# Performance work log

Hardware: AMD Instinct MI355X
Metric: run time of the kernel (lower is better)

## Reference

```python
import jax, jax.numpy as jnp
import numpy as np

H = 128  # hidden_size
I = 28   # input_size
C = 10   # num_classes


def setup_inputs() -> dict:
    key = jax.random.key(0)
    ks = jax.random.split(key, 11)
    s = 1.0 / np.sqrt(H)  # torch nn.RNN init scale
    return {
        "x": jax.random.normal(ks[0], (8192, 28, I), dtype=jnp.float32),
        "W_ih0": jax.random.uniform(ks[1], (H, I), jnp.float32, -s, s),
        "W_hh0": jax.random.uniform(ks[2], (H, H), jnp.float32, -s, s),
        "b_ih0": jax.random.uniform(ks[3], (H,), jnp.float32, -s, s),
        "b_hh0": jax.random.uniform(ks[4], (H,), jnp.float32, -s, s),
        "W_ih1": jax.random.uniform(ks[5], (H, H), jnp.float32, -s, s),
        "W_hh1": jax.random.uniform(ks[6], (H, H), jnp.float32, -s, s),
        "b_ih1": jax.random.uniform(ks[7], (H,), jnp.float32, -s, s),
        "b_hh1": jax.random.uniform(ks[8], (H,), jnp.float32, -s, s),
        "fc_w": jax.random.uniform(ks[9], (C, H), jnp.float32, -s, s),
        "fc_b": jax.random.uniform(ks[10], (C,), jnp.float32, -s, s),
    }


def _rnn_layer_full(x, W_ih, b_ih, W_hh, b_hh):
    # x: [B, T, D] -> full output sequence [B, T, H]
    B = x.shape[0]
    h0 = jnp.zeros((B, H), x.dtype)
    xw = jnp.einsum('btd,hd->bth', x, W_ih) + b_ih  # precompute input GEMM

    def step(h, xw_t):
        h = jnp.tanh(xw_t + h @ W_hh.T + b_hh)
        return h, h

    _, ys = jax.lax.scan(step, h0, jnp.swapaxes(xw, 0, 1))  # [T, B, H]
    return jnp.swapaxes(ys, 0, 1)


def _rnn_layer_last(x, W_ih, b_ih, W_hh, b_hh):
    # only the final hidden state is needed downstream
    B = x.shape[0]
    h0 = jnp.zeros((B, H), x.dtype)
    xw = jnp.einsum('btd,hd->bth', x, W_ih) + b_ih

    def step(h, xw_t):
        h = jnp.tanh(xw_t + h @ W_hh.T + b_hh)
        return h, None

    h_last, _ = jax.lax.scan(step, h0, jnp.swapaxes(xw, 0, 1))
    return h_last


def reference(x, W_ih0, W_hh0, b_ih0, b_hh0, W_ih1, W_hh1, b_ih1, b_hh1, fc_w, fc_b):
    out0 = _rnn_layer_full(x, W_ih0, b_ih0, W_hh0, b_hh0)   # [B, T, H]
    h_last = _rnn_layer_last(out0, W_ih1, b_ih1, W_hh1, b_hh1)  # [B, H] == out[:, -1, :]
    return h_last @ fc_w.T + fc_b  # [B, C]
```

## Files before the change

### kernel.cpp

```cpp
#include <hip/hip_runtime.h>

#define HSZ 128
#define ISZ 28
#define TSZ 28
#define CSZ 10
#define BT  32
#define NG  2
#define NT  384

typedef _Float16 half_t;
typedef _Float16 v8h __attribute__((ext_vector_type(8)));
typedef _Float16 v4h __attribute__((ext_vector_type(4)));
typedef float v4f __attribute__((ext_vector_type(4)));

__device__ __forceinline__ float fast_tanh(float x) {
    float e = __expf(2.f * x);
    return 1.f - 2.f * __builtin_amdgcn_rcpf(e + 1.f);
}
__device__ __forceinline__ int imin(int a, int b) { return a < b ? a : b; }

__global__ __launch_bounds__(NT, 2)
void rnn_ws(const float* __restrict__ x,
            const float* __restrict__ W_ih0, const float* __restrict__ W_hh0,
            const float* __restrict__ b_ih0, const float* __restrict__ b_hh0,
            const float* __restrict__ W_ih1, const float* __restrict__ W_hh1,
            const float* __restrict__ b_ih1, const float* __restrict__ b_hh1,
            const float* __restrict__ fc_w, const float* __restrict__ fc_b,
            float* __restrict__ out)
{
    __shared__ half_t xs[TSZ][NG][512];
    __shared__ half_t h0r[4][NG][2048];
    __shared__ half_t h1r[4][NG][2048];
    __shared__ int    flags[8];

    const int tid  = threadIdx.x;
    const int wave = tid >> 6;
    const int lane = tid & 63;
    const int ln   = lane & 15;
    const int quad = lane >> 4;
    const int b0   = blockIdx.x * BT;
    const int ro   = lane * 8;
    const int wbq  = (quad >> 1) * 128 + ln * 8 + (quad & 1) * 4;
    volatile int* vf = (volatile int*)flags;

    for (int it = 0; it < 10; ++it) {
        const int c = tid + it * NT;
        if (c < TSZ * 128) {
            const int q = c & 3;
            const int n = (c >> 2) & 15;
            const int g = (c >> 6) & 1;
            const int t = c >> 7;
            const float* gp = x + ((size_t)(b0 + g * 16 + n) * TSZ + t) * ISZ + q * 8;
            float4 a = *(const float4*)gp;
            float4 b = (q < 3) ? *(const float4*)(gp + 4) : make_float4(1.f, 0.f, 0.f, 0.f);
            v8h p = {(half_t)a.x, (half_t)a.y, (half_t)a.z, (half_t)a.w,
                     (half_t)b.x, (half_t)b.y, (half_t)b.z, (half_t)b.w};
            *(v8h*)&xs[t][g][(q * 16 + n) * 8] = p;
        }
    }
    {
        const v8h z = {(half_t)0.f, (half_t)0.f, (half_t)0.f, (half_t)0.f,
                       (half_t)0.f, (half_t)0.f, (half_t)0.f, (half_t)0.f};
        for (int idx = tid; idx < 512; idx += NT) {
            *(v8h*)&h0r[3][0][idx * 8] = z;
            *(v8h*)&h1r[3][0][idx * 8] = z;
        }
        if (tid < 8) flags[tid] = 0;
    }
    __syncthreads();

    if (wave < NG) {
        const int g = wave;
        v8h aWx[8], aW0[8][4];
#pragma unroll
        for (int rt = 0; rt < 8; ++rt) {
            const int row = rt * 16 + ln;
            const float bias = b_ih0[row] + b_hh0[row];
            const float* pw = W_ih0 + row * ISZ + quad * 8;
            float4 a = *(const float4*)pw;
            float4 b = (quad < 3) ? *(const float4*)(pw + 4)
                                  : make_float4(bias, 0.f, 0.f, 0.f);
            aWx[rt] = (v8h){(half_t)a.x, (half_t)a.y, (half_t)a.z, (half_t)a.w,
                            (half_t)b.x, (half_t)b.y, (half_t)b.z, (half_t)b.w};
#pragma unroll
            for (int ks = 0; ks < 4; ++ks) {
                const float4* p0 = (const float4*)(W_hh0 + row * HSZ + ks * 32 + quad * 8);
                float4 c = p0[0], d = p0[1];
                aW0[rt][ks] = (v8h){(half_t)c.x, (half_t)c.y, (half_t)c.z, (half_t)c.w,
                                    (half_t)d.x, (half_t)d.y, (half_t)d.z, (half_t)d.w};
            }
        }
        __builtin_amdgcn_s_setprio(1);

        for (int t = 0; t < TSZ; ++t) {
            if (t >= 4) {
                while (imin(vf[2 + 2 * g], vf[3 + 2 * g]) < t - 3)
                    __builtin_amdgcn_s_sleep(1);
            }
            __asm__ volatile("" ::: "memory");
            const int sr = (t + 3) & 3, sw = t & 3;

            v8h bh[4];
#pragma unroll
            for (int ks = 0; ks < 4; ++ks)
                bh[ks] = *(const v8h*)&h0r[sr][g][ks * 512 + ro];
            const v8h bx = *(const v8h*)&xs[t][g][ro];

            v4f acc[8];
#pragma unroll
            for (int rt = 0; rt < 8; ++rt)
                acc[rt] = __builtin_amdgcn_mfma_f32_16x16x32_f16(
                    aWx[rt], bx, (v4f){0.f, 0.f, 0.f, 0.f}, 0, 0, 0);
#pragma unroll
            for (int ks = 0; ks < 4; ++ks)
#pragma unroll
                for (int rt = 0; rt < 8; ++rt)
                    acc[rt] = __builtin_amdgcn_mfma_f32_16x16x32_f16(
                        aW0[rt][ks], bh[ks], acc[rt], 0, 0, 0);
#pragma unroll
            for (int rt = 0; rt < 8; ++rt) {
                v4h p = {(half_t)fast_tanh(acc[rt][0]), (half_t)fast_tanh(acc[rt][1]),
                         (half_t)fast_tanh(acc[rt][2]), (half_t)fast_tanh(acc[rt][3])};
                *(v4h*)&h0r[sw][g][(rt >> 1) * 512 + (rt & 1) * 256 + wbq] = p;
            }
            __asm__ volatile("s_waitcnt lgkmcnt(0)" ::: "memory");
            if (lane == 0) vf[g] = t + 1;
        }
        __builtin_amdgcn_s_setprio(0);
    } else {
        const int q4 = wave - 2;
        const int g  = q4 >> 1;
        const int c  = q4 & 1;
        v8h aW1i[4][4], aW1h[4][4];
        v4f bias1[4];
#pragma unroll
        for (int rt = 0; rt < 4; ++rt) {
            const int row = c * 64 + rt * 16 + ln;
            float4 p = *(const float4*)(b_ih1 + c * 64 + rt * 16 + quad * 4);
            float4 q = *(const float4*)(b_hh1 + c * 64 + rt * 16 + quad * 4);
            bias1[rt] = (v4f){p.x + q.x, p.y + q.y, p.z + q.z, p.w + q.w};
#pragma unroll
            for (int ks = 0; ks < 4; ++ks) {
                const float4* p1 = (const float4*)(W_ih1 + row * HSZ + ks * 32 + quad * 8);
                const float4* p2 = (const float4*)(W_hh1 + row * HSZ + ks * 32 + quad * 8);
                float4 a = p1[0], b = p1[1];
                aW1i[rt][ks] = (v8h){(half_t)a.x, (half_t)a.y, (half_t)a.z, (half_t)a.w,
                                     (half_t)b.x, (half_t)b.y, (half_t)b.z, (half_t)b.w};
                a = p2[0]; b = p2[1];
                aW1h[rt][ks] = (v8h){(half_t)a.x, (half_t)a.y, (half_t)a.z, (half_t)a.w,
                                     (half_t)b.x, (half_t)b.y, (half_t)b.z, (half_t)b.w};
            }
        }

        for (int t = 0; t < TSZ; ++t) {
            const int pid = 2 + 2 * g + (c ^ 1);
            while (vf[g] < t + 1 || vf[pid] < t)
                __builtin_amdgcn_s_sleep(1);
            __asm__ volatile("" ::: "memory");
            const int s0 = t & 3, s1 = (t + 3) & 3;

            v8h bh0[4], bh1[4];
#pragma unroll
            for (int ks = 0; ks < 4; ++ks) {
                bh0[ks] = *(const v8h*)&h0r[s0][g][ks * 512 + ro];
                bh1[ks] = *(const v8h*)&h1r[s1][g][ks * 512 + ro];
            }
            v4f si[4], sh[4];
#pragma unroll
            for (int rt = 0; rt < 4; ++rt) {
                si[rt] = bias1[rt];
                sh[rt] = (v4f){0.f, 0.f, 0.f, 0.f};
            }
#pragma unroll
            for (int ks = 0; ks < 4; ++ks)
#pragma unroll
                for (int rt = 0; rt < 4; ++rt) {
                    si[rt] = __builtin_amdgcn_mfma_f32_16x16x32_f16(
                        aW1i[rt][ks], bh0[ks], si[rt], 0, 0, 0);
                    sh[rt] = __builtin_amdgcn_mfma_f32_16x16x32_f16(
                        aW1h[rt][ks], bh1[ks], sh[rt], 0, 0, 0);
                }
#pragma unroll
            for (int rt = 0; rt < 4; ++rt) {
                const v4f a1 = si[rt] + sh[rt];
                const int rtg = c * 4 + rt;
                v4h p = {(half_t)fast_tanh(a1[0]), (half_t)fast_tanh(a1[1]),
                         (half_t)fast_tanh(a1[2]), (half_t)fast_tanh(a1[3])};
                *(v4h*)&h1r[s0][g][(rtg >> 1) * 512 + (rtg & 1) * 256 + wbq] = p;
            }
            __asm__ volatile("s_waitcnt lgkmcnt(0)" ::: "memory");
            if (lane == 0) vf[2 + 2 * g + c] = t + 1;
        }
    }
    __syncthreads();

    if (tid < BT * CSZ) {
        const int m = tid / CSZ, cc = tid - m * CSZ;
        const int g = m >> 4, n = m & 15;
        float s = fc_b[cc];
#pragma unroll
        for (int ks = 0; ks < 4; ++ks) {
#pragma unroll
            for (int q2 = 0; q2 < 4; ++q2) {
                const v8h hv = *(const v8h*)&h1r[3][g][(ks * 64 + q2 * 16 + n) * 8];
                const int kb = ks * 32 + q2 * 8;
                const float4 w0 = *(const float4*)(fc_w + cc * HSZ + kb);
                const float4 w1 = *(const float4*)(fc_w + cc * HSZ + kb + 4);
                s += (float)hv[0] * w0.x + (float)hv[1] * w0.y +
                     (float)hv[2] * w0.z + (float)hv[3] * w0.w +
                     (float)hv[4] * w1.x + (float)hv[5] * w1.y +
                     (float)hv[6] * w1.z + (float)hv[7] * w1.w;
            }
        }
        out[(b0 + m) * CSZ + cc] = s;
    }
}

extern "C" void kernel_launch(void* const* d_in, const int* in_sizes, int n_in,
                              void* d_out, int out_size, void* d_ws, size_t ws_size,
                              hipStream_t stream) {
    const float* x     = (const float*)d_in[0];
    const float* W_ih0 = (const float*)d_in[1];
    const float* W_hh0 = (const float*)d_in[2];
    const float* b_ih0 = (const float*)d_in[3];
    const float* b_hh0 = (const float*)d_in[4];
    const float* W_ih1 = (const float*)d_in[5];
    const float* W_hh1 = (const float*)d_in[6];
    const float* b_ih1 = (const float*)d_in[7];
    const float* b_hh1 = (const float*)d_in[8];
    const float* fc_w  = (const float*)d_in[9];
    const float* fc_b  = (const float*)d_in[10];
    float* out = (float*)d_out;

    const int B = in_sizes[0] / (TSZ * ISZ);
    dim3 grid(B / BT), block(NT);
    rnn_ws<<<grid, block, 0, stream>>>(x, W_ih0, W_hh0, b_ih0, b_hh0,
                                       W_ih1, W_hh1, b_ih1, b_hh1,
                                       fc_w, fc_b, out);
}
```

Measured before the change: 152.8 us.

## Replace warp-specialized flag-synced RNN with single-wave block per 16 batch rows

```diff
diff --git a/kernel.cpp b/kernel.cpp
--- a/kernel.cpp
+++ b/kernel.cpp
@@ -4,9 +4,8 @@
 #define ISZ 28
 #define TSZ 28
 #define CSZ 10
-#define BT  32
-#define NG  2
-#define NT  384
+#define BT  16
+#define NT  64
 
 typedef _Float16 half_t;
 typedef _Float16 v8h __attribute__((ext_vector_type(8)));
@@ -17,192 +16,152 @@
     float e = __expf(2.f * x);
     return 1.f - 2.f * __builtin_amdgcn_rcpf(e + 1.f);
 }
-__device__ __forceinline__ int imin(int a, int b) { return a < b ? a : b; }
 
-__global__ __launch_bounds__(NT, 2)
-void rnn_ws(const float* __restrict__ x,
-            const float* __restrict__ W_ih0, const float* __restrict__ W_hh0,
-            const float* __restrict__ b_ih0, const float* __restrict__ b_hh0,
-            const float* __restrict__ W_ih1, const float* __restrict__ W_hh1,
-            const float* __restrict__ b_ih1, const float* __restrict__ b_hh1,
-            const float* __restrict__ fc_w, const float* __restrict__ fc_b,
-            float* __restrict__ out)
+__global__ __launch_bounds__(NT, 1)
+void rnn_zsync(const float* __restrict__ x,
+               const float* __restrict__ W_ih0, const float* __restrict__ W_hh0,
+               const float* __restrict__ b_ih0, const float* __restrict__ b_hh0,
+               const float* __restrict__ W_ih1, const float* __restrict__ W_hh1,
+               const float* __restrict__ b_ih1, const float* __restrict__ b_hh1,
+               const float* __restrict__ fc_w, const float* __restrict__ fc_b,
+               float* __restrict__ out)
 {
-    __shared__ half_t xs[TSZ][NG][512];
-    __shared__ half_t h0r[4][NG][2048];
-    __shared__ half_t h1r[4][NG][2048];
-    __shared__ int    flags[8];
+    __shared__ half_t xs[TSZ][512];
+    __shared__ half_t aWxL[8 * 512];
+    __shared__ half_t h0b[2048];
+    __shared__ half_t h1b[2048];
 
-    const int tid  = threadIdx.x;
-    const int wave = tid >> 6;
-    const int lane = tid & 63;
+    const int lane = threadIdx.x;
     const int ln   = lane & 15;
     const int quad = lane >> 4;
     const int b0   = blockIdx.x * BT;
     const int ro   = lane * 8;
     const int wbq  = (quad >> 1) * 128 + ln * 8 + (quad & 1) * 4;
-    volatile int* vf = (volatile int*)flags;
 
-    for (int it = 0; it < 10; ++it) {
-        const int c = tid + it * NT;
-        if (c < TSZ * 128) {
-            const int q = c & 3;
-            const int n = (c >> 2) & 15;
-            const int g = (c >> 6) & 1;
-            const int t = c >> 7;
-            const float* gp = x + ((size_t)(b0 + g * 16 + n) * TSZ + t) * ISZ + q * 8;
-            float4 a = *(const float4*)gp;
-            float4 b = (q < 3) ? *(const float4*)(gp + 4) : make_float4(1.f, 0.f, 0.f, 0.f);
-            v8h p = {(half_t)a.x, (half_t)a.y, (half_t)a.z, (half_t)a.w,
-                     (half_t)b.x, (half_t)b.y, (half_t)b.z, (half_t)b.w};
-            *(v8h*)&xs[t][g][(q * 16 + n) * 8] = p;
-        }
-    }
-    {
-        const v8h z = {(half_t)0.f, (half_t)0.f, (half_t)0.f, (half_t)0.f,
-                       (half_t)0.f, (half_t)0.f, (half_t)0.f, (half_t)0.f};
-        for (int idx = tid; idx < 512; idx += NT) {
-            *(v8h*)&h0r[3][0][idx * 8] = z;
-            *(v8h*)&h1r[3][0][idx * 8] = z;
-        }
-        if (tid < 8) flags[tid] = 0;
-    }
-    __syncthreads();
+    v8h aW0[8][4], aW1i[8][4], aW1h[8][4];
+    v4h bias1h[8];
 
-    if (wave < NG) {
-        const int g = wave;
-        v8h aWx[8], aW0[8][4];
 #pragma unroll
-        for (int rt = 0; rt < 8; ++rt) {
-            const int row = rt * 16 + ln;
+    for (int rt = 0; rt < 8; ++rt) {
+        const int row = rt * 16 + ln;
+        {
             const float bias = b_ih0[row] + b_hh0[row];
             const float* pw = W_ih0 + row * ISZ + quad * 8;
             float4 a = *(const float4*)pw;
             float4 b = (quad < 3) ? *(const float4*)(pw + 4)
                                   : make_float4(bias, 0.f, 0.f, 0.f);
-            aWx[rt] = (v8h){(half_t)a.x, (half_t)a.y, (half_t)a.z, (half_t)a.w,
-                            (half_t)b.x, (half_t)b.y, (half_t)b.z, (half_t)b.w};
+            v8h f = {(half_t)a.x, (half_t)a.y, (half_t)a.z, (half_t)a.w,
+                     (half_t)b.x, (half_t)b.y, (half_t)b.z, (half_t)b.w};
+            *(v8h*)&aWxL[rt * 512 + ro] = f;
+        }
+        {
+            float4 p = *(const float4*)(b_ih1 + rt * 16 + quad * 4);
+            float4 q = *(const float4*)(b_hh1 + rt * 16 + quad * 4);
+            bias1h[rt] = (v4h){(half_t)(p.x + q.x), (half_t)(p.y + q.y),
+                               (half_t)(p.z + q.z), (half_t)(p.w + q.w)};
+        }
 #pragma unroll
-            for (int ks = 0; ks < 4; ++ks) {
-                const float4* p0 = (const float4*)(W_hh0 + row * HSZ + ks * 32 + quad * 8);
-                float4 c = p0[0], d = p0[1];
-                aW0[rt][ks] = (v8h){(half_t)c.x, (half_t)c.y, (half_t)c.z, (half_t)c.w,
-                                    (half_t)d.x, (half_t)d.y, (half_t)d.z, (half_t)d.w};
-            }
+        for (int ks = 0; ks < 4; ++ks) {
+            const float4* p0 = (const float4*)(W_hh0 + row * HSZ + ks * 32 + quad * 8);
+            const float4* p1 = (const float4*)(W_ih1 + row * HSZ + ks * 32 + quad * 8);
+            const float4* p2 = (const float4*)(W_hh1 + row * HSZ + ks * 32 + quad * 8);
+            float4 a = p0[0], b = p0[1];
+            aW0[rt][ks] = (v8h){(half_t)a.x, (half_t)a.y, (half_t)a.z, (half_t)a.w,
+                                (half_t)b.x, (half_t)b.y, (half_t)b.z, (half_t)b.w};
+            a = p1[0]; b = p1[1];
+            aW1i[rt][ks] = (v8h){(half_t)a.x, (half_t)a.y, (half_t)a.z, (half_t)a.w,
+                                 (half_t)b.x, (half_t)b.y, (half_t)b.z, (half_t)b.w};
+            a = p2[0]; b = p2[1];
+            aW1h[rt][ks] = (v8h){(half_t)a.x, (half_t)a.y, (half_t)a.z, (half_t)a.w,
+                                 (half_t)b.x, (half_t)b.y, (half_t)b.z, (half_t)b.w};
         }
-        __builtin_amdgcn_s_setprio(1);
+    }
 
-        for (int t = 0; t < TSZ; ++t) {
-            if (t >= 4) {
-                while (imin(vf[2 + 2 * g], vf[3 + 2 * g]) < t - 3)
-                    __builtin_amdgcn_s_sleep(1);
-            }
-            __asm__ volatile("" ::: "memory");
-            const int sr = (t + 3) & 3, sw = t & 3;
+#pragma unroll
+    for (int it = 0; it < 28; ++it) {
+        const int c = lane + it * NT;
+        const int q = c & 3;
+        const int n = (c >> 2) & 15;
+        const int t = c >> 6;
+        const float* gp = x + ((size_t)(b0 + n) * TSZ + t) * ISZ + q * 8;
+        float4 a = *(const float4*)gp;
+        float4 b = (q < 3) ? *(const float4*)(gp + 4) : make_float4(1.f, 0.f, 0.f, 0.f);
+        v8h p = {(half_t)a.x, (half_t)a.y, (half_t)a.z, (half_t)a.w,
+                 (half_t)b.x, (half_t)b.y, (half_t)b.z, (half_t)b.w};
+        *(v8h*)&xs[t][(q * 16 + n) * 8] = p;
+    }
+    {
+        const v8h z = {(half_t)0.f, (half_t)0.f, (half_t)0.f, (half_t)0.f,
+                       (half_t)0.f, (half_t)0.f, (half_t)0.f, (half_t)0.f};
+#pragma unroll
+        for (int i = 0; i < 4; ++i) {
+            *(v8h*)&h0b[(i * 64 + lane) * 8] = z;
+            *(v8h*)&h1b[(i * 64 + lane) * 8] = z;
+        }
+    }
 
-            v8h bh[4];
+    int tof = 0;
+    for (int t = 0; t < TSZ; ++t) {
+        asm volatile("" : "+v"(tof));
+
+        const v8h bx = *(const v8h*)&xs[t][ro];
+        v4f acc[8];
 #pragma unroll
-            for (int ks = 0; ks < 4; ++ks)
-                bh[ks] = *(const v8h*)&h0r[sr][g][ks * 512 + ro];
-            const v8h bx = *(const v8h*)&xs[t][g][ro];
-
-            v4f acc[8];
+        for (int rt = 0; rt < 8; ++rt)
+            acc[rt] = __builtin_amdgcn_mfma_f32_16x16x32_f16(
+                *(const v8h*)&aWxL[rt * 512 + ro + tof], bx,
+                (v4f){0.f, 0.f, 0.f, 0.f}, 0, 0, 0);
+#pragma unroll
+        for (int ks = 0; ks < 4; ++ks) {
+            const v8h bh = *(const v8h*)&h0b[ks * 512 + ro];
 #pragma unroll
             for (int rt = 0; rt < 8; ++rt)
                 acc[rt] = __builtin_amdgcn_mfma_f32_16x16x32_f16(
-                    aWx[rt], bx, (v4f){0.f, 0.f, 0.f, 0.f}, 0, 0, 0);
+                    aW0[rt][ks], bh, acc[rt], 0, 0, 0);
+        }
 #pragma unroll
-            for (int ks = 0; ks < 4; ++ks)
-#pragma unroll
-                for (int rt = 0; rt < 8; ++rt)
-                    acc[rt] = __builtin_amdgcn_mfma_f32_16x16x32_f16(
-                        aW0[rt][ks], bh[ks], acc[rt], 0, 0, 0);
-#pragma unroll
-            for (int rt = 0; rt < 8; ++rt) {
-                v4h p = {(half_t)fast_tanh(acc[rt][0]), (half_t)fast_tanh(acc[rt][1]),
-                         (half_t)fast_tanh(acc[rt][2]), (half_t)fast_tanh(acc[rt][3])};
-                *(v4h*)&h0r[sw][g][(rt >> 1) * 512 + (rt & 1) * 256 + wbq] = p;
-            }
-            __asm__ volatile("s_waitcnt lgkmcnt(0)" ::: "memory");
-            if (lane == 0) vf[g] = t + 1;
-        }
-        __builtin_amdgcn_s_setprio(0);
-    } else {
-        const int q4 = wave - 2;
-        const int g  = q4 >> 1;
-        const int c  = q4 & 1;
-        v8h aW1i[4][4], aW1h[4][4];
-        v4f bias1[4];
-#pragma unroll
-        for (int rt = 0; rt < 4; ++rt) {
-            const int row = c * 64 + rt * 16 + ln;
-            float4 p = *(const float4*)(b_ih1 + c * 64 + rt * 16 + quad * 4);
-            float4 q = *(const float4*)(b_hh1 + c * 64 + rt * 16 + quad * 4);
-            bias1[rt] = (v4f){p.x + q.x, p.y + q.y, p.z + q.z, p.w + q.w};
-#pragma unroll
-            for (int ks = 0; ks < 4; ++ks) {
-                const float4* p1 = (const float4*)(W_ih1 + row * HSZ + ks * 32 + quad * 8);
-                const float4* p2 = (const float4*)(W_hh1 + row * HSZ + ks * 32 + quad * 8);
-                float4 a = p1[0], b = p1[1];
-                aW1i[rt][ks] = (v8h){(half_t)a.x, (half_t)a.y, (half_t)a.z, (half_t)a.w,
-                                     (half_t)b.x, (half_t)b.y, (half_t)b.z, (half_t)b.w};
-                a = p2[0]; b = p2[1];
-                aW1h[rt][ks] = (v8h){(half_t)a.x, (half_t)a.y, (half_t)a.z, (half_t)a.w,
-                                     (half_t)b.x, (half_t)b.y, (half_t)b.z, (half_t)b.w};
-            }
+        for (int rt = 0; rt < 8; ++rt) {
+            v4h p = {(half_t)fast_tanh(acc[rt][0]), (half_t)fast_tanh(acc[rt][1]),
+                     (half_t)fast_tanh(acc[rt][2]), (half_t)fast_tanh(acc[rt][3])};
+            *(v4h*)&h0b[(rt >> 1) * 512 + (rt & 1) * 256 + wbq] = p;
         }
 
-        for (int t = 0; t < TSZ; ++t) {
-            const int pid = 2 + 2 * g + (c ^ 1);
-            while (vf[g] < t + 1 || vf[pid] < t)
-                __builtin_amdgcn_s_sleep(1);
-            __asm__ volatile("" ::: "memory");
-            const int s0 = t & 3, s1 = (t + 3) & 3;
-
-            v8h bh0[4], bh1[4];
 #pragma unroll
-            for (int ks = 0; ks < 4; ++ks) {
-                bh0[ks] = *(const v8h*)&h0r[s0][g][ks * 512 + ro];
-                bh1[ks] = *(const v8h*)&h1r[s1][g][ks * 512 + ro];
-            }
-            v4f si[4], sh[4];
+        for (int rt = 0; rt < 8; ++rt)
+            acc[rt] = (v4f){(float)bias1h[rt][0], (float)bias1h[rt][1],
+                            (float)bias1h[rt][2], (float)bias1h[rt][3]};
 #pragma unroll
-            for (int rt = 0; rt < 4; ++rt) {
-                si[rt] = bias1[rt];
-                sh[rt] = (v4f){0.f, 0.f, 0.f, 0.f};
-            }
+        for (int ks = 0; ks < 4; ++ks) {
+            const v8h bh1o = *(const v8h*)&h1b[ks * 512 + ro];
 #pragma unroll
-            for (int ks = 0; ks < 4; ++ks)
+            for (int rt = 0; rt < 8; ++rt)
+                acc[rt] = __builtin_amdgcn_mfma_f32_16x16x32_f16(
+                    aW1h[rt][ks], bh1o, acc[rt], 0, 0, 0);
+        }
 #pragma unroll
-                for (int rt = 0; rt < 4; ++rt) {
-                    si[rt] = __builtin_amdgcn_mfma_f32_16x16x32_f16(
-                        aW1i[rt][ks], bh0[ks], si[rt], 0, 0, 0);
-                    sh[rt] = __builtin_amdgcn_mfma_f32_16x16x32_f16(
-                        aW1h[rt][ks], bh1[ks], sh[rt], 0, 0, 0);
-                }
+        for (int ks = 0; ks < 4; ++ks) {
+            const v8h bh0n = *(const v8h*)&h0b[ks * 512 + ro];
 #pragma unroll
-            for (int rt = 0; rt < 4; ++rt) {
-                const v4f a1 = si[rt] + sh[rt];
-                const int rtg = c * 4 + rt;
-                v4h p = {(half_t)fast_tanh(a1[0]), (half_t)fast_tanh(a1[1]),
-                         (half_t)fast_tanh(a1[2]), (half_t)fast_tanh(a1[3])};
-                *(v4h*)&h1r[s0][g][(rtg >> 1) * 512 + (rtg & 1) * 256 + wbq] = p;
-            }
-            __asm__ volatile("s_waitcnt lgkmcnt(0)" ::: "memory");
-            if (lane == 0) vf[2 + 2 * g + c] = t + 1;
+            for (int rt = 0; rt < 8; ++rt)
+                acc[rt] = __builtin_amdgcn_mfma_f32_16x16x32_f16(
+                    aW1i[rt][ks], bh0n, acc[rt], 0, 0, 0);
+        }
+#pragma unroll
+        for (int rt = 0; rt < 8; ++rt) {
+            v4h p = {(half_t)fast_tanh(acc[rt][0]), (half_t)fast_tanh(acc[rt][1]),
+                     (half_t)fast_tanh(acc[rt][2]), (half_t)fast_tanh(acc[rt][3])};
+            *(v4h*)&h1b[(rt >> 1) * 512 + (rt & 1) * 256 + wbq] = p;
         }
     }
-    __syncthreads();
 
-    if (tid < BT * CSZ) {
-        const int m = tid / CSZ, cc = tid - m * CSZ;
-        const int g = m >> 4, n = m & 15;
+    for (int p = lane; p < BT * CSZ; p += NT) {
+        const int m = p / CSZ, cc = p - m * CSZ;
         float s = fc_b[cc];
 #pragma unroll
         for (int ks = 0; ks < 4; ++ks) {
 #pragma unroll
             for (int q2 = 0; q2 < 4; ++q2) {
-                const v8h hv = *(const v8h*)&h1r[3][g][(ks * 64 + q2 * 16 + n) * 8];
+                const v8h hv = *(const v8h*)&h1b[(ks * 64 + q2 * 16 + m) * 8];
                 const int kb = ks * 32 + q2 * 8;
                 const float4 w0 = *(const float4*)(fc_w + cc * HSZ + kb);
                 const float4 w1 = *(const float4*)(fc_w + cc * HSZ + kb + 4);
@@ -234,7 +193,7 @@
 
     const int B = in_sizes[0] / (TSZ * ISZ);
     dim3 grid(B / BT), block(NT);
-    rnn_ws<<<grid, block, 0, stream>>>(x, W_ih0, W_hh0, b_ih0, b_hh0,
-                                       W_ih1, W_hh1, b_ih1, b_hh1,
-                                       fc_w, fc_b, out);
+    rnn_zsync<<<grid, block, 0, stream>>>(x, W_ih0, W_hh0, b_ih0, b_hh0,
+                                          W_ih1, W_hh1, b_ih1, b_hh1,
+                                          fc_w, fc_b, out);
 }
```

After: 231.3 us. 51.4% more time.
